# Kernel optimization log

Measured on AMD Instinct MI355X. Metric: run time of the kernel, lower is better.

The kernel has to match this reference:

```python
import jax, jax.numpy as jnp
import numpy as np

RES = 128        # 2**base_lod, base_lod=7, num_lod=1
FEAT_DIM = 18


def setup_inputs() -> dict:
    key = jax.random.key(0)
    k1, k2 = jax.random.split(key)
    pts = jax.random.uniform(k1, (4, 524288, 3), dtype=jnp.float32)
    codebook = jax.random.normal(k2, (RES ** 3, FEAT_DIM), dtype=jnp.float32) * 0.01
    transform = jnp.eye(4, dtype=jnp.float32)
    return {"pts": pts, "codebook": codebook, "transform": transform}


def _trilinear(res, codebook, pts):
    # pts: [N,3] in [0,1]; NGLOD-style dense grid trilinear interpolation
    p = pts * (res - 1)
    p0 = jnp.floor(p)
    w = p - p0                                   # [N,3] fractional weights
    i0 = jnp.clip(p0.astype(jnp.int32), 0, res - 1)
    i1 = jnp.clip(i0 + 1, 0, res - 1)
    feats = jnp.zeros((pts.shape[0], codebook.shape[1]), dtype=codebook.dtype)
    for dz in (0, 1):
        iz = (i1 if dz else i0)[:, 2]
        wz = w[:, 2] if dz else 1.0 - w[:, 2]
        for dy in (0, 1):
            iy = (i1 if dy else i0)[:, 1]
            wy = w[:, 1] if dy else 1.0 - w[:, 1]
            for dx in (0, 1):
                ix = (i1 if dx else i0)[:, 0]
                wx = w[:, 0] if dx else 1.0 - w[:, 0]
                idx = ix + iy * res + iz * res * res   # x + y*res + z*res^2
                feats = feats + codebook[idx] * (wx * wy * wz)[:, None]
    return feats


def reference(pts, codebook, transform):
    # flatten 'b h c -> (b h) c'
    p = pts.reshape(-1, 3)
    R_inv = jnp.linalg.inv(transform[:3, :3])
    p = (R_inv @ (p.T - transform[:3, 3:4])).T
    feats = _trilinear(RES, codebook, p)
    # single LOD: cat over lod axis then sum(-1) is identity
    return feats
```

## Files before the change

kernel.cpp:

```cpp
#include <hip/hip_runtime.h>


constexpr int RES  = 128;
constexpr int NBA  = 512;
constexpr int TPM  = 576;
constexpr int PPB  = 64;
constexpr int SUB_CAP = 8160;

constexpr int HIST_CHUNK = 1024;
constexpr int SCAT_CHUNK = 16384;

typedef float vf2 __attribute__((ext_vector_type(2)));
typedef float vf4 __attribute__((ext_vector_type(4)));

struct Xf {
    float m00, m01, m02, m10, m11, m12, m20, m21, m22;
    float tx, ty, tz;
};

__device__ __forceinline__ Xf load_xf(const float* __restrict__ tr) {
    Xf X;
    const float a = tr[0], b = tr[1],  c = tr[2];
    const float d = tr[4], e = tr[5],  g = tr[6];
    const float h = tr[8], i = tr[9],  j = tr[10];
    X.tx = tr[3]; X.ty = tr[7]; X.tz = tr[11];
    const float det = a*(e*j - g*i) - b*(d*j - g*h) + c*(d*i - e*h);
    const float rd  = 1.0f / det;
    X.m00 = (e*j - g*i) * rd; X.m01 = (c*i - b*j) * rd; X.m02 = (b*g - c*e) * rd;
    X.m10 = (g*h - d*j) * rd; X.m11 = (a*j - c*h) * rd; X.m12 = (c*d - a*g) * rd;
    X.m20 = (d*i - e*h) * rd; X.m21 = (b*h - a*i) * rd; X.m22 = (a*e - b*d) * rd;
    return X;
}

__device__ __forceinline__ float qcoord(float m0, float m1, float m2,
                                        float x, float y, float z) {
    return __fmaf_rn(m0, x, __fmaf_rn(m1, y, m2 * z)) * (float)(RES - 1);
}

__device__ __forceinline__ int clamp_idx(float q) {
    return min(max((int)floorf(q), 0), RES - 1);
}

__device__ __forceinline__ int coarse_key(float qy, float qz) {
    return (clamp_idx(qz) << 2) | (clamp_idx(qy) >> 5);
}

__global__ __launch_bounds__(256)
void k_zero(unsigned* __restrict__ histA) {
    const int i = blockIdx.x * 256 + threadIdx.x;
    if (i < NBA) histA[i] = 0u;
}

__global__ __launch_bounds__(256)
void k_histA(const float* __restrict__ pts, const float* __restrict__ tr,
             unsigned* __restrict__ histA, int npts)
{
    __shared__ unsigned sh[NBA];
    const int t = threadIdx.x;
    for (int b = t; b < NBA; b += 256) sh[b] = 0u;
    __syncthreads();
    const Xf X = load_xf(tr);
    const int base = blockIdx.x * HIST_CHUNK;
    #pragma unroll
    for (int i = 0; i < HIST_CHUNK / 256; ++i) {
        const int p = base + t + i * 256;
        if (p < npts) {
            const float x = pts[p*3 + 0] - X.tx;
            const float y = pts[p*3 + 1] - X.ty;
            const float z = pts[p*3 + 2] - X.tz;
            const float qy = qcoord(X.m10, X.m11, X.m12, x, y, z);
            const float qz = qcoord(X.m20, X.m21, X.m22, x, y, z);
            atomicAdd(&sh[coarse_key(qy, qz)], 1u);
        }
    }
    __syncthreads();
    for (int b = t; b < NBA; b += 256) {
        const unsigned c = sh[b];
        if (c) atomicAdd(&histA[b], c);
    }
}

__global__ __launch_bounds__(NBA)
void k_scanA(const unsigned* __restrict__ histA,
             unsigned* __restrict__ baseA, unsigned* __restrict__ cursorA)
{
    __shared__ unsigned s[NBA];
    const int t = threadIdx.x;
    const unsigned my = histA[t];
    s[t] = my;
    __syncthreads();
    for (int off = 1; off < NBA; off <<= 1) {
        const unsigned v = (t >= off) ? s[t - off] : 0u;
        __syncthreads();
        s[t] += v;
        __syncthreads();
    }
    baseA[t]   = s[t] - my;
    cursorA[t] = s[t] - my;
}

__global__ __launch_bounds__(256)
void k_scatA(const float* __restrict__ pts, const float* __restrict__ tr,
             unsigned* __restrict__ cursorA, vf4* __restrict__ rec, int npts)
{
    __shared__ unsigned shist[NBA], sbase[NBA], scur[NBA];
    const int t = threadIdx.x;
    for (int b = t; b < NBA; b += 256) { shist[b] = 0u; scur[b] = 0u; }
    __syncthreads();
    const Xf X = load_xf(tr);
    const int base = blockIdx.x * SCAT_CHUNK;
    for (int i = 0; i < SCAT_CHUNK / 256; ++i) {
        const int p = base + t + i * 256;
        if (p < npts) {
            const float x = pts[p*3 + 0] - X.tx;
            const float y = pts[p*3 + 1] - X.ty;
            const float z = pts[p*3 + 2] - X.tz;
            const float qy = qcoord(X.m10, X.m11, X.m12, x, y, z);
            const float qz = qcoord(X.m20, X.m21, X.m22, x, y, z);
            atomicAdd(&shist[coarse_key(qy, qz)], 1u);
        }
    }
    __syncthreads();
    for (int b = t; b < NBA; b += 256)
        sbase[b] = shist[b] ? atomicAdd(&cursorA[b], shist[b]) : 0u;
    __syncthreads();
    for (int i = 0; i < SCAT_CHUNK / 256; ++i) {
        const int p = base + t + i * 256;
        if (p < npts) {
            const float x = pts[p*3 + 0] - X.tx;
            const float y = pts[p*3 + 1] - X.ty;
            const float z = pts[p*3 + 2] - X.tz;
            const float qx = qcoord(X.m00, X.m01, X.m02, x, y, z);
            const float qy = qcoord(X.m10, X.m11, X.m12, x, y, z);
            const float qz = qcoord(X.m20, X.m21, X.m22, x, y, z);
            const int bn = coarse_key(qy, qz);
            const unsigned r = atomicAdd(&scur[bn], 1u);
            unsigned pos = sbase[bn] + r;
            if (pos >= (unsigned)npts) pos = (unsigned)npts - 1u;
            vf4 v; v.x = qx; v.y = qy; v.z = qz; v.w = __int_as_float(p);
            rec[pos] = v;
        }
    }
}

__global__ __launch_bounds__(1024)
void k_subsort(vf4* __restrict__ rec, const unsigned* __restrict__ histA,
               const unsigned* __restrict__ baseA)
{
    const int cbn = blockIdx.x;
    const int t = threadIdx.x;
    const unsigned n = histA[cbn];
    const unsigned b0 = baseA[cbn];
    const int ybase = (cbn & 3) << 5;

    if (n == 0u || n > (unsigned)SUB_CAP) return;

    __shared__ vf4 c[SUB_CAP];
    __shared__ unsigned h[256], cur[256];
    for (int k = t; k < 256; k += 1024) h[k] = 0u;
    __syncthreads();

    for (unsigned i = t; i < n; i += 1024) {
        const vf4 v = rec[b0 + i];
        c[i] = v;
        const int ky = min(max(clamp_idx(v.y) - ybase, 0), 31);
        const int kx = clamp_idx(v.x) >> 4;
        atomicAdd(&h[(ky << 3) | kx], 1u);
    }
    __syncthreads();
    if (t == 0) {
        unsigned run = 0u;
        for (int k = 0; k < 256; ++k) { cur[k] = run; run += h[k]; }
    }
    __syncthreads();
    for (unsigned i = t; i < n; i += 1024) {
        const vf4 v = c[i];
        const int ky = min(max(clamp_idx(v.y) - ybase, 0), 31);
        const int kx = clamp_idx(v.x) >> 4;
        const unsigned pos = atomicAdd(&cur[(ky << 3) | kx], 1u);
        rec[b0 + pos] = v;
    }
}

__global__ __launch_bounds__(TPM)
void k_main6(const vf4* __restrict__ rec, const float* __restrict__ cb,
             float* __restrict__ out, int npts, int nwg)
{
    const int bid = blockIdx.x;
    const int q = nwg >> 3, r = nwg & 7;
    const int xcd = bid & 7, lin = bid >> 3;
    const int blk = (xcd < r ? xcd * (q + 1) : r * (q + 1) + (xcd - r) * q) + lin;

    __shared__ vf4 srec[PPB];
    const int t = threadIdx.x;
    const int g0 = blk * PPB;
    if (t < PPB) {
        const int g = g0 + t;
        if (g < npts) srec[t] = __builtin_nontemporal_load(&rec[g]);
    }
    __syncthreads();

    const int pl = t / 9;
    const int f  = t - pl * 9;
    const int p  = g0 + pl;
    if (p >= npts) return;

    const vf4 rr = srec[pl];
    const float qx = rr.x, qy = rr.y, qz = rr.z;
    const int idx = __float_as_int(rr.w);

    const float fx = floorf(qx), fy = floorf(qy), fz = floorf(qz);
    const float wx1 = qx - fx, wy1 = qy - fy, wz1 = qz - fz;
    const float wx0 = 1.0f - wx1, wy0 = 1.0f - wy1, wz0 = 1.0f - wz1;
    const int ix0 = clamp_idx(qx); const int ix1 = min(ix0 + 1, RES - 1);
    const int iy0 = clamp_idx(qy); const int iy1 = min(iy0 + 1, RES - 1);
    const int iz0 = clamp_idx(qz); const int iz1 = min(iz0 + 1, RES - 1);

    int   ro[8];
    float w[8];
    #pragma unroll
    for (int k = 0; k < 8; ++k) {
        const int dx = k & 1, dy = (k >> 1) & 1, dz = k >> 2;
        ro[k] = (dx ? ix1 : ix0) + ((dy ? iy1 : iy0) << 7) + ((dz ? iz1 : iz0) << 14);
        w[k]  = (dx ? wx1 : wx0) * (dy ? wy1 : wy0) * (dz ? wz1 : wz0);
    }

    const float* cbf = cb + 2 * f;
    vf2 v[8];
    #pragma unroll
    for (int k = 0; k < 8; ++k)
        v[k] = *reinterpret_cast<const vf2*>(cbf + (size_t)ro[k] * 18);

    float ax = 0.0f, ay = 0.0f;
    #pragma unroll
    for (int k = 0; k < 8; ++k) { ax += v[k].x * w[k]; ay += v[k].y * w[k]; }

    vf2 o; o.x = ax; o.y = ay;
    __builtin_nontemporal_store(o, reinterpret_cast<vf2*>(out + (size_t)idx * 18 + 2 * f));
}

__global__ __launch_bounds__(TPM)
void dense_grid_trilerp(const float* __restrict__ pts,
                        const float* __restrict__ cb,
                        const float* __restrict__ tr,
                        float* __restrict__ out,
                        int npts)
{
    __shared__ float spts[PPB * 3];
    if (threadIdx.x < PPB * 3) {
        int g = blockIdx.x * (PPB * 3) + threadIdx.x;
        spts[threadIdx.x] = (g < npts * 3) ? __builtin_nontemporal_load(&pts[g]) : 0.0f;
    }
    __syncthreads();

    const int pl = threadIdx.x / 9;
    const int f  = threadIdx.x - pl * 9;
    const int p  = blockIdx.x * PPB + pl;
    if (p >= npts) return;

    const Xf X = load_xf(tr);
    const float x = spts[pl*3 + 0] - X.tx;
    const float y = spts[pl*3 + 1] - X.ty;
    const float z = spts[pl*3 + 2] - X.tz;
    const float qx = qcoord(X.m00, X.m01, X.m02, x, y, z);
    const float qy = qcoord(X.m10, X.m11, X.m12, x, y, z);
    const float qz = qcoord(X.m20, X.m21, X.m22, x, y, z);

    const float fx = floorf(qx), fy = floorf(qy), fz = floorf(qz);
    const float wx1 = qx - fx, wy1 = qy - fy, wz1 = qz - fz;
    const float wx0 = 1.0f - wx1, wy0 = 1.0f - wy1, wz0 = 1.0f - wz1;
    const int ix0 = clamp_idx(qx); const int ix1 = min(ix0 + 1, RES - 1);
    const int iy0 = clamp_idx(qy); const int iy1 = min(iy0 + 1, RES - 1);
    const int iz0 = clamp_idx(qz); const int iz1 = min(iz0 + 1, RES - 1);

    int   ro[8];
    float w[8];
    #pragma unroll
    for (int k = 0; k < 8; ++k) {
        const int dx = k & 1, dy = (k >> 1) & 1, dz = k >> 2;
        ro[k] = (dx ? ix1 : ix0) + ((dy ? iy1 : iy0) << 7) + ((dz ? iz1 : iz0) << 14);
        w[k]  = (dx ? wx1 : wx0) * (dy ? wy1 : wy0) * (dz ? wz1 : wz0);
    }

    const float* cbf = cb + 2 * f;
    vf2 v[8];
    #pragma unroll
    for (int k = 0; k < 8; ++k)
        v[k] = *reinterpret_cast<const vf2*>(cbf + (size_t)ro[k] * 18);

    float ax = 0.0f, ay = 0.0f;
    #pragma unroll
    for (int k = 0; k < 8; ++k) { ax += v[k].x * w[k]; ay += v[k].y * w[k]; }

    vf2 o; o.x = ax; o.y = ay;
    __builtin_nontemporal_store(o, reinterpret_cast<vf2*>(out + p * 18 + 2 * f));
}

extern "C" void kernel_launch(void* const* d_in, const int* in_sizes, int n_in,
                              void* d_out, int out_size, void* d_ws, size_t ws_size,
                              hipStream_t stream) {
    const float* pts = (const float*)d_in[0];
    const float* cb  = (const float*)d_in[1];
    const float* tr  = (const float*)d_in[2];
    float* out = (float*)d_out;

    const int npts = in_sizes[0] / 3;

    const size_t meta = (size_t)(NBA * 3) * sizeof(unsigned);
    const size_t need = meta + (size_t)npts * 16;
    if (d_ws == nullptr || ws_size < need || npts <= 0) {
        const int blocks = (npts + PPB - 1) / PPB;
        dense_grid_trilerp<<<blocks, TPM, 0, stream>>>(pts, cb, tr, out, npts);
        return;
    }

    unsigned* histA   = (unsigned*)d_ws;
    unsigned* baseA   = histA + NBA;
    unsigned* cursorA = baseA + NBA;
    vf4* rec = (vf4*)((char*)d_ws + meta);

    const int nwg = (npts + PPB - 1) / PPB;
    k_zero<<<(NBA + 255) / 256, 256, 0, stream>>>(histA);
    k_histA<<<(npts + HIST_CHUNK - 1) / HIST_CHUNK, 256, 0, stream>>>(pts, tr, histA, npts);
    k_scanA<<<1, NBA, 0, stream>>>(histA, baseA, cursorA);
    k_scatA<<<(npts + SCAT_CHUNK - 1) / SCAT_CHUNK, 256, 0, stream>>>(pts, tr, cursorA, rec, npts);
    k_subsort<<<NBA, 1024, 0, stream>>>(rec, histA, baseA);
    k_main6<<<nwg, TPM, 0, stream>>>(rec, cb, out, npts, nwg);
}
```

Measured before the change: 523.7 us.

## Fuse subsort with trilinear gather and write sorted features then unsort

Doubles the coarse bin count, so each bin covers a z slice and 16 y rows. The local sort is fused with the trilinear interpolation in one per-bin kernel that reorders through a shared-memory index array instead of writing records back. Features are written in sorted order to a workspace buffer along with an inverse permutation. A separate unsort kernel then copies them to the output with coalesced writes. This trades the scattered output writes for an extra 72-byte-per-point round trip, and bins larger than the shared capacity fall back to an unsorted path.

```diff
diff --git a/kernel.cpp b/kernel.cpp
--- a/kernel.cpp
+++ b/kernel.cpp
@@ -2,13 +2,13 @@
 
 
 constexpr int RES  = 128;
-constexpr int NBA  = 512;
+constexpr int NBA  = 1024;
 constexpr int TPM  = 576;
 constexpr int PPB  = 64;
-constexpr int SUB_CAP = 8160;
+constexpr int SUB_CAP = 3264;
 
 constexpr int HIST_CHUNK = 1024;
-constexpr int SCAT_CHUNK = 16384;
+constexpr int SCAT_CHUNK = 4096;
 
 typedef float vf2 __attribute__((ext_vector_type(2)));
 typedef float vf4 __attribute__((ext_vector_type(4)));
@@ -42,13 +42,7 @@
 }
 
 __device__ __forceinline__ int coarse_key(float qy, float qz) {
-    return (clamp_idx(qz) << 2) | (clamp_idx(qy) >> 5);
-}
-
-__global__ __launch_bounds__(256)
-void k_zero(unsigned* __restrict__ histA) {
-    const int i = blockIdx.x * 256 + threadIdx.x;
-    if (i < NBA) histA[i] = 0u;
+    return (clamp_idx(qz) << 3) | (clamp_idx(qy) >> 4);
 }
 
 __global__ __launch_bounds__(256)
@@ -109,6 +103,7 @@
     __syncthreads();
     const Xf X = load_xf(tr);
     const int base = blockIdx.x * SCAT_CHUNK;
+    #pragma unroll
     for (int i = 0; i < SCAT_CHUNK / 256; ++i) {
         const int p = base + t + i * 256;
         if (p < npts) {
@@ -124,6 +119,7 @@
     for (int b = t; b < NBA; b += 256)
         sbase[b] = shist[b] ? atomicAdd(&cursorA[b], shist[b]) : 0u;
     __syncthreads();
+    #pragma unroll
     for (int i = 0; i < SCAT_CHUNK / 256; ++i) {
         const int p = base + t + i * 256;
         if (p < npts) {
@@ -143,61 +139,105 @@
     }
 }
 
-__global__ __launch_bounds__(1024)
-void k_subsort(vf4* __restrict__ rec, const unsigned* __restrict__ histA,
-               const unsigned* __restrict__ baseA)
-{
-    const int cbn = blockIdx.x;
-    const int t = threadIdx.x;
-    const unsigned n = histA[cbn];
-    const unsigned b0 = baseA[cbn];
-    const int ybase = (cbn & 3) << 5;
-
-    if (n == 0u || n > (unsigned)SUB_CAP) return;
-
-    __shared__ vf4 c[SUB_CAP];
-    __shared__ unsigned h[256], cur[256];
-    for (int k = t; k < 256; k += 1024) h[k] = 0u;
-    __syncthreads();
-
-    for (unsigned i = t; i < n; i += 1024) {
-        const vf4 v = rec[b0 + i];
-        c[i] = v;
-        const int ky = min(max(clamp_idx(v.y) - ybase, 0), 31);
+__global__ __launch_bounds__(TPM)
+void k_fused(const vf4* __restrict__ rec, const unsigned* __restrict__ histA,
+             const unsigned* __restrict__ baseA, const float* __restrict__ cb,
+             float* __restrict__ feat_s, unsigned* __restrict__ inv,
+             float* __restrict__ out, int direct)
+{
+    const int bid = blockIdx.x;
+    const int bin = (bid & 7) * (NBA / 8) + (bid >> 3);
+
+    const unsigned n  = histA[bin];
+    if (n == 0u) return;
+    const unsigned b0 = baseA[bin];
+    const int ybase = (bin & 7) << 4;
+
+    const int t  = threadIdx.x;
+    const int pl = t / 9;
+    const int f  = t - pl * 9;
+
+    __shared__ vf4 recs[SUB_CAP];
+    __shared__ unsigned short ord[SUB_CAP];
+    __shared__ unsigned h[128], cur[128];
+
+    auto emit = [&](const vf4 r, unsigned spos) {
+        const float qx = r.x, qy = r.y, qz = r.z;
+        const int idx = __float_as_int(r.w);
+        const float fx = floorf(qx), fy = floorf(qy), fz = floorf(qz);
+        const float wx1 = qx - fx, wy1 = qy - fy, wz1 = qz - fz;
+        const float wx0 = 1.0f - wx1, wy0 = 1.0f - wy1, wz0 = 1.0f - wz1;
+        const int ix0 = clamp_idx(qx), ix1 = min(ix0 + 1, RES - 1);
+        const int iy0 = clamp_idx(qy), iy1 = min(iy0 + 1, RES - 1);
+        const int iz0 = clamp_idx(qz), iz1 = min(iz0 + 1, RES - 1);
+        vf2 v[8]; float w[8];
+        #pragma unroll
+        for (int k = 0; k < 8; ++k) {
+            const int dx = k & 1, dy = (k >> 1) & 1, dz = k >> 2;
+            const int ro = (dx ? ix1 : ix0) + ((dy ? iy1 : iy0) << 7)
+                         + ((dz ? iz1 : iz0) << 14);
+            v[k] = *reinterpret_cast<const vf2*>(cb + (size_t)ro * 18 + 2 * f);
+            w[k] = (dx ? wx1 : wx0) * (dy ? wy1 : wy0) * (dz ? wz1 : wz0);
+        }
+        float ax = 0.0f, ay = 0.0f;
+        #pragma unroll
+        for (int k = 0; k < 8; ++k) { ax += v[k].x * w[k]; ay += v[k].y * w[k]; }
+        vf2 o; o.x = ax; o.y = ay;
+        if (direct) {
+            __builtin_nontemporal_store(o,
+                reinterpret_cast<vf2*>(out + (size_t)idx * 18 + 2 * f));
+        } else {
+            *reinterpret_cast<vf2*>(feat_s + (size_t)spos * 18 + 2 * f) = o;
+            if (f == 0) inv[idx] = spos;
+        }
+    };
+
+    if (n > (unsigned)SUB_CAP) {
+        for (unsigned off = 0; off < n; off += PPB) {
+            const unsigned i = off + (unsigned)pl;
+            if (i < n) emit(__builtin_nontemporal_load(&rec[b0 + i]), b0 + i);
+        }
+        return;
+    }
+
+    for (int k = t; k < 128; k += TPM) h[k] = 0u;
+    __syncthreads();
+    for (unsigned i = t; i < n; i += TPM) {
+        const vf4 v = __builtin_nontemporal_load(&rec[b0 + i]);
+        recs[i] = v;
+        const int ky = min(max(clamp_idx(v.y) - ybase, 0), 15);
         const int kx = clamp_idx(v.x) >> 4;
         atomicAdd(&h[(ky << 3) | kx], 1u);
     }
     __syncthreads();
     if (t == 0) {
         unsigned run = 0u;
-        for (int k = 0; k < 256; ++k) { cur[k] = run; run += h[k]; }
-    }
-    __syncthreads();
-    for (unsigned i = t; i < n; i += 1024) {
-        const vf4 v = c[i];
-        const int ky = min(max(clamp_idx(v.y) - ybase, 0), 31);
+        for (int k = 0; k < 128; ++k) { cur[k] = run; run += h[k]; }
+    }
+    __syncthreads();
+    for (unsigned i = t; i < n; i += TPM) {
+        const vf4 v = recs[i];
+        const int ky = min(max(clamp_idx(v.y) - ybase, 0), 15);
         const int kx = clamp_idx(v.x) >> 4;
-        const unsigned pos = atomicAdd(&cur[(ky << 3) | kx], 1u);
-        rec[b0 + pos] = v;
+        ord[atomicAdd(&cur[(ky << 3) | kx], 1u)] = (unsigned short)i;
+    }
+    __syncthreads();
+
+    for (unsigned off = 0; off < n; off += PPB) {
+        const unsigned i = off + (unsigned)pl;
+        if (i < n) emit(recs[ord[i]], b0 + i);
     }
 }
 
 __global__ __launch_bounds__(TPM)
-void k_main6(const vf4* __restrict__ rec, const float* __restrict__ cb,
-             float* __restrict__ out, int npts, int nwg)
-{
-    const int bid = blockIdx.x;
-    const int q = nwg >> 3, r = nwg & 7;
-    const int xcd = bid & 7, lin = bid >> 3;
-    const int blk = (xcd < r ? xcd * (q + 1) : r * (q + 1) + (xcd - r) * q) + lin;
-
-    __shared__ vf4 srec[PPB];
+void k_unsort(const float* __restrict__ feat_s, const unsigned* __restrict__ inv,
+              float* __restrict__ out, int npts)
+{
+    __shared__ unsigned sinv[PPB];
     const int t = threadIdx.x;
-    const int g0 = blk * PPB;
-    if (t < PPB) {
-        const int g = g0 + t;
-        if (g < npts) srec[t] = __builtin_nontemporal_load(&rec[g]);
-    }
+    const int g0 = blockIdx.x * PPB;
+    if (t < PPB && g0 + t < npts)
+        sinv[t] = __builtin_nontemporal_load(&inv[g0 + t]);
     __syncthreads();
 
     const int pl = t / 9;
@@ -205,38 +245,10 @@
     const int p  = g0 + pl;
     if (p >= npts) return;
 
-    const vf4 rr = srec[pl];
-    const float qx = rr.x, qy = rr.y, qz = rr.z;
-    const int idx = __float_as_int(rr.w);
-
-    const float fx = floorf(qx), fy = floorf(qy), fz = floorf(qz);
-    const float wx1 = qx - fx, wy1 = qy - fy, wz1 = qz - fz;
-    const float wx0 = 1.0f - wx1, wy0 = 1.0f - wy1, wz0 = 1.0f - wz1;
-    const int ix0 = clamp_idx(qx); const int ix1 = min(ix0 + 1, RES - 1);
-    const int iy0 = clamp_idx(qy); const int iy1 = min(iy0 + 1, RES - 1);
-    const int iz0 = clamp_idx(qz); const int iz1 = min(iz0 + 1, RES - 1);
-
-    int   ro[8];
-    float w[8];
-    #pragma unroll
-    for (int k = 0; k < 8; ++k) {
-        const int dx = k & 1, dy = (k >> 1) & 1, dz = k >> 2;
-        ro[k] = (dx ? ix1 : ix0) + ((dy ? iy1 : iy0) << 7) + ((dz ? iz1 : iz0) << 14);
-        w[k]  = (dx ? wx1 : wx0) * (dy ? wy1 : wy0) * (dz ? wz1 : wz0);
-    }
-
-    const float* cbf = cb + 2 * f;
-    vf2 v[8];
-    #pragma unroll
-    for (int k = 0; k < 8; ++k)
-        v[k] = *reinterpret_cast<const vf2*>(cbf + (size_t)ro[k] * 18);
-
-    float ax = 0.0f, ay = 0.0f;
-    #pragma unroll
-    for (int k = 0; k < 8; ++k) { ax += v[k].x * w[k]; ay += v[k].y * w[k]; }
-
-    vf2 o; o.x = ax; o.y = ay;
-    __builtin_nontemporal_store(o, reinterpret_cast<vf2*>(out + (size_t)idx * 18 + 2 * f));
+    const unsigned s = sinv[pl];
+    const vf2 v = *reinterpret_cast<const vf2*>(feat_s + (size_t)s * 18 + 2 * f);
+    __builtin_nontemporal_store(v,
+        reinterpret_cast<vf2*>(out + (size_t)p * 18 + 2 * f));
 }
 
 __global__ __launch_bounds__(TPM)
@@ -306,9 +318,14 @@
 
     const int npts = in_sizes[0] / 3;
 
-    const size_t meta = (size_t)(NBA * 3) * sizeof(unsigned);
-    const size_t need = meta + (size_t)npts * 16;
-    if (d_ws == nullptr || ws_size < need || npts <= 0) {
+    const size_t meta      = (size_t)(NBA * 3) * sizeof(unsigned);
+    const size_t rec_b     = (size_t)npts * 16;
+    const size_t inv_b     = (size_t)npts * 4;
+    const size_t feat_b    = (size_t)npts * 72;
+    const size_t need_mid  = meta + rec_b;
+    const size_t need_full = meta + rec_b + inv_b + feat_b;
+
+    if (d_ws == nullptr || ws_size < need_mid || npts <= 0) {
         const int blocks = (npts + PPB - 1) / PPB;
         dense_grid_trilerp<<<blocks, TPM, 0, stream>>>(pts, cb, tr, out, npts);
         return;
@@ -317,13 +334,16 @@
     unsigned* histA   = (unsigned*)d_ws;
     unsigned* baseA   = histA + NBA;
     unsigned* cursorA = baseA + NBA;
-    vf4* rec = (vf4*)((char*)d_ws + meta);
-
-    const int nwg = (npts + PPB - 1) / PPB;
-    k_zero<<<(NBA + 255) / 256, 256, 0, stream>>>(histA);
+    vf4*      rec     = (vf4*)((char*)d_ws + meta);
+    unsigned* inv     = (unsigned*)((char*)d_ws + meta + rec_b);
+    float*    feat_s  = (float*)((char*)d_ws + meta + rec_b + inv_b);
+    const int full    = (ws_size >= need_full) ? 1 : 0;
+
+    hipMemsetAsync(histA, 0, meta, stream);
     k_histA<<<(npts + HIST_CHUNK - 1) / HIST_CHUNK, 256, 0, stream>>>(pts, tr, histA, npts);
     k_scanA<<<1, NBA, 0, stream>>>(histA, baseA, cursorA);
     k_scatA<<<(npts + SCAT_CHUNK - 1) / SCAT_CHUNK, 256, 0, stream>>>(pts, tr, cursorA, rec, npts);
-    k_subsort<<<NBA, 1024, 0, stream>>>(rec, histA, baseA);
-    k_main6<<<nwg, TPM, 0, stream>>>(rec, cb, out, npts, nwg);
-}
+    k_fused<<<NBA, TPM, 0, stream>>>(rec, histA, baseA, cb, feat_s, inv, out, full ? 0 : 1);
+    if (full)
+        k_unsort<<<(npts + PPB - 1) / PPB, TPM, 0, stream>>>(feat_s, inv, out, npts);
+}
```

After: 580.3 us. 10.8% more time.
